# Kernel optimization log

Hardware: AMD Instinct MI355X
Metric: run time of the kernel (lower is better)

## Reference

```python
import jax, jax.numpy as jnp
import numpy as np

N_NODES = 100000
N_EDGES = 1200000
IN_DIM = 64
HID = 64
N_GRAPHS = 512
N_CLASSES = 1
LN_EPS = 1e-5
NORM_EPS = 1e-12


def _layer_norm(x, g, b):
    mu = x.mean(-1, keepdims=True)
    var = ((x - mu) ** 2).mean(-1, keepdims=True)
    return (x - mu) * jax.lax.rsqrt(var + LN_EPS) * g + b


def setup_inputs() -> dict:
    key = jax.random.key(0)
    ks = jax.random.split(key, 20)
    h = jax.random.normal(ks[0], (N_NODES, IN_DIM), jnp.float32)
    src = jax.random.randint(ks[1], (N_EDGES,), 0, N_NODES)
    dst = jax.random.randint(ks[2], (N_EDGES,), 0, N_NODES)
    graph_ids = jnp.sort(jax.random.randint(ks[3], (N_NODES,), 0, N_GRAPHS))
    s1 = 1.0 / np.sqrt(IN_DIM)
    s2 = 1.0 / np.sqrt(HID)
    s3 = 1.0 / np.sqrt(2 * HID)
    return {
        "h": h, "src": src, "dst": dst, "graph_ids": graph_ids,
        "W1": jax.random.normal(ks[4], (IN_DIM, HID), jnp.float32) * s1,
        "b1": jnp.zeros((HID,), jnp.float32),
        "W2": jax.random.normal(ks[5], (HID, HID), jnp.float32) * s2,
        "b2": jnp.zeros((HID,), jnp.float32),
        "g1": jnp.ones((HID,), jnp.float32), "be1": jnp.zeros((HID,), jnp.float32),
        "g2": jnp.ones((HID,), jnp.float32), "be2": jnp.zeros((HID,), jnp.float32),
        "g3": jnp.ones((HID,), jnp.float32), "be3": jnp.zeros((HID,), jnp.float32),
        "g4": jnp.ones((HID,), jnp.float32), "be4": jnp.zeros((HID,), jnp.float32),
        "Wc1": jax.random.normal(ks[6], (2 * HID, HID), jnp.float32) * s3,
        "bc1": jnp.zeros((HID,), jnp.float32),
        "Wc2": jax.random.normal(ks[7], (HID, HID), jnp.float32) * s2,
        "bc2": jnp.zeros((HID,), jnp.float32),
        "Wc3": jax.random.normal(ks[8], (HID, N_CLASSES), jnp.float32) * s2,
        "bc3": jnp.zeros((N_CLASSES,), jnp.float32),
    }


def reference(h, src, dst, graph_ids, W1, b1, W2, b2, g1, be1, g2, be2,
              g3, be3, g4, be4, Wc1, bc1, Wc2, bc2, Wc3, bc3):
    N = N_NODES
    ones_e = jnp.ones((src.shape[0],), jnp.float32)
    # DGL GraphConv norm='both': symmetric degree normalization (clamp 0 -> 1)
    deg_out = jnp.clip(jax.ops.segment_sum(ones_e, src, num_segments=N), 1.0)
    deg_in = jnp.clip(jax.ops.segment_sum(ones_e, dst, num_segments=N), 1.0)
    ns = (deg_out ** -0.5)[:, None]
    nd = (deg_in ** -0.5)[:, None]

    def conv(x, W, b):
        msg = (x * ns)[src]                                  # [E, d] gather
        agg = jax.ops.segment_sum(msg, dst, num_segments=N)  # [N, d] scatter-add
        return (agg * nd) @ W + b

    h1 = jax.nn.relu(_layer_norm(conv(h, W1, b1), g1, be1))
    h1 = jax.nn.relu(_layer_norm(conv(h1, W2, b2), g2, be2))

    # per-graph mean / max pooling (dgl.mean_nodes / dgl.max_nodes)
    ssum = jax.ops.segment_sum(h1, graph_ids, num_segments=N_GRAPHS)
    cnt = jnp.clip(jax.ops.segment_sum(jnp.ones((N,), jnp.float32), graph_ids,
                                       num_segments=N_GRAPHS), 1.0)
    hg = ssum / cnt[:, None]
    hg_max = jax.ops.segment_max(h1, graph_ids, num_segments=N_GRAPHS)

    def l2norm(x):  # F.normalize(p=2, dim=1)
        n = jnp.sqrt((x * x).sum(-1, keepdims=True))
        return x / jnp.maximum(n, NORM_EPS)

    hg = jnp.concatenate([l2norm(hg), l2norm(hg_max)], axis=1)  # [G, 2*HID]
    out = jax.nn.relu(_layer_norm(hg @ Wc1 + bc1, g3, be3))
    out = jax.nn.relu(_layer_norm(out @ Wc2 + bc2, g4, be4))
    return out @ Wc3 + bc3
```

## Files before the change

kernel.cpp:

```cpp
#include <hip/hip_runtime.h>
#include <math.h>

#define HID 64
#define LN_EPS 1e-5f
#define NORM_EPS 1e-12f
#define CHUNK 1024
#define CONV_BLOCKS 2048

typedef _Float16 half4v __attribute__((ext_vector_type(4)));

__device__ __forceinline__ float wave_sum64(float v) {
#pragma unroll
    for (int o = 32; o > 0; o >>= 1) v += __shfl_xor(v, o, 64);
    return v;
}

__device__ __forceinline__ int lower_bound_dev(const int* __restrict__ a, int n, int key) {
    int lo = 0, hi = n;
    while (lo < hi) {
        int mid = (lo + hi) >> 1;
        if (a[mid] < key) lo = mid + 1; else hi = mid;
    }
    return lo;
}

__global__ __launch_bounds__(256) void count_kernel(const int* __restrict__ src,
                                                    const int* __restrict__ dst,
                                                    int* __restrict__ cnt_out,
                                                    int* __restrict__ cnt_in,
                                                    int E) {
    int e0 = (blockIdx.x * 256 + threadIdx.x) * 4;
    if (e0 + 3 < E) {
        int4 s4 = *reinterpret_cast<const int4*>(src + e0);
        int4 d4 = *reinterpret_cast<const int4*>(dst + e0);
        atomicAdd(&cnt_out[s4.x], 1); atomicAdd(&cnt_out[s4.y], 1);
        atomicAdd(&cnt_out[s4.z], 1); atomicAdd(&cnt_out[s4.w], 1);
        atomicAdd(&cnt_in[d4.x], 1);  atomicAdd(&cnt_in[d4.y], 1);
        atomicAdd(&cnt_in[d4.z], 1);  atomicAdd(&cnt_in[d4.w], 1);
    } else {
        for (int e = e0; e < E; ++e) {
            atomicAdd(&cnt_out[src[e]], 1);
            atomicAdd(&cnt_in[dst[e]], 1);
        }
    }
}

__global__ __launch_bounds__(256) void scan1_kernel(const int* __restrict__ cnt_in,
                                                    const int* __restrict__ cnt_out,
                                                    float* __restrict__ ns,
                                                    float* __restrict__ nd,
                                                    int* __restrict__ cs,
                                                    int* __restrict__ partials,
                                                    int N) {
    __shared__ int wsum[4];
    int t = threadIdx.x;
    int lane = t & 63, wave = t >> 6;
    int base = blockIdx.x * CHUNK + t * 4;
    int v0 = (base + 0 < N) ? cnt_in[base + 0] : 0;
    int v1 = (base + 1 < N) ? cnt_in[base + 1] : 0;
    int v2 = (base + 2 < N) ? cnt_in[base + 2] : 0;
    int v3 = (base + 3 < N) ? cnt_in[base + 3] : 0;

    if (base + 3 < N) {
        int4 co = *reinterpret_cast<const int4*>(cnt_out + base);
        float4 nsv = make_float4(rsqrtf((float)max(co.x, 1)), rsqrtf((float)max(co.y, 1)),
                                 rsqrtf((float)max(co.z, 1)), rsqrtf((float)max(co.w, 1)));
        float4 ndv = make_float4(rsqrtf((float)max(v0, 1)), rsqrtf((float)max(v1, 1)),
                                 rsqrtf((float)max(v2, 1)), rsqrtf((float)max(v3, 1)));
        *reinterpret_cast<float4*>(ns + base) = nsv;
        *reinterpret_cast<float4*>(nd + base) = ndv;
    } else {
        for (int i = base; i < N; ++i) {
            ns[i] = rsqrtf((float)max(cnt_out[i], 1));
            nd[i] = rsqrtf((float)max(cnt_in[i], 1));
        }
    }

    int tsum = v0 + v1 + v2 + v3;
    int x = tsum;
#pragma unroll
    for (int off = 1; off < 64; off <<= 1) {
        int y = __shfl_up(x, off, 64);
        if (lane >= off) x += y;
    }
    if (lane == 63) wsum[wave] = x;
    __syncthreads();
    int waveoff = 0;
    for (int w = 0; w < wave; ++w) waveoff += wsum[w];
    int off0 = waveoff + x - tsum;
    if (base + 0 < N) cs[base + 0] = off0;
    if (base + 1 < N) cs[base + 1] = off0 + v0;
    if (base + 2 < N) cs[base + 2] = off0 + v0 + v1;
    if (base + 3 < N) cs[base + 3] = off0 + v0 + v1 + v2;
    if (t == 255) partials[blockIdx.x] = waveoff + x;
}

__global__ __launch_bounds__(256) void scan2_kernel(int* __restrict__ partials, int nch) {
    __shared__ int wsum[4];
    int t = threadIdx.x;
    int lane = t & 63, wave = t >> 6;
    int base = t * 4;
    int v0 = (base + 0 < nch) ? partials[base + 0] : 0;
    int v1 = (base + 1 < nch) ? partials[base + 1] : 0;
    int v2 = (base + 2 < nch) ? partials[base + 2] : 0;
    int v3 = (base + 3 < nch) ? partials[base + 3] : 0;
    int tsum = v0 + v1 + v2 + v3;
    int x = tsum;
#pragma unroll
    for (int off = 1; off < 64; off <<= 1) {
        int y = __shfl_up(x, off, 64);
        if (lane >= off) x += y;
    }
    if (lane == 63) wsum[wave] = x;
    __syncthreads();
    int waveoff = 0;
    for (int w = 0; w < wave; ++w) waveoff += wsum[w];
    int off0 = waveoff + x - tsum;
    if (base + 0 < nch) partials[base + 0] = off0;
    if (base + 1 < nch) partials[base + 1] = off0 + v0;
    if (base + 2 < nch) partials[base + 2] = off0 + v0 + v1;
    if (base + 3 < nch) partials[base + 3] = off0 + v0 + v1 + v2;
}

__global__ __launch_bounds__(256) void scan3_kernel(int* __restrict__ cs,
                                                    const int* __restrict__ partials,
                                                    int* __restrict__ cursor,
                                                    int N, int E) {
    int n = blockIdx.x * 256 + threadIdx.x;
    if (n < N) {
        int v = cs[n] + partials[n / CHUNK];
        cs[n] = v;
        cursor[n] = v;
    }
    if (n == 0) cs[N] = E;
}

__global__ __launch_bounds__(256) void prescale_kernel(const float* __restrict__ x,
                                                       const float* __restrict__ ns,
                                                       _Float16* __restrict__ xs,
                                                       int total) {
    int i = (blockIdx.x * 256 + threadIdx.x) * 4;
    if (i >= total) return;
    float w = ns[i >> 6];
    float4 v = *reinterpret_cast<const float4*>(x + i);
    half4v o;
    o.x = (_Float16)(v.x * w);
    o.y = (_Float16)(v.y * w);
    o.z = (_Float16)(v.z * w);
    o.w = (_Float16)(v.w * w);
    *reinterpret_cast<half4v*>(xs + i) = o;
}

__global__ __launch_bounds__(256) void fill_kernel(const int* __restrict__ src,
                                                   const int* __restrict__ dst,
                                                   int* __restrict__ cursor,
                                                   int* __restrict__ eidx,
                                                   int E) {
    int e0 = (blockIdx.x * 256 + threadIdx.x) * 4;
    if (e0 + 3 < E) {
        int4 s4 = *reinterpret_cast<const int4*>(src + e0);
        int4 d4 = *reinterpret_cast<const int4*>(dst + e0);
        int p0 = atomicAdd(&cursor[d4.x], 1);
        int p1 = atomicAdd(&cursor[d4.y], 1);
        int p2 = atomicAdd(&cursor[d4.z], 1);
        int p3 = atomicAdd(&cursor[d4.w], 1);
        eidx[p0] = s4.x;
        eidx[p1] = s4.y;
        eidx[p2] = s4.z;
        eidx[p3] = s4.w;
    } else {
        for (int e = e0; e < E; ++e) {
            int p = atomicAdd(&cursor[dst[e]], 1);
            eidx[p] = src[e];
        }
    }
}

template <int MODE>
__global__ __launch_bounds__(256, 8) void conv_kernel(const _Float16* __restrict__ xs,
                                                      const int* __restrict__ eidx,
                                                      const int* __restrict__ cs,
                                                      const float* __restrict__ nd,
                                                      const float* __restrict__ ns,
                                                      const float* __restrict__ W,
                                                      const float* __restrict__ b,
                                                      const float* __restrict__ gam,
                                                      const float* __restrict__ bet,
                                                      void* __restrict__ outp,
                                                      int N) {
    __shared__ float Ws[HID * HID];
    int tid = threadIdx.x;
#pragma unroll
    for (int i = tid; i < HID * HID / 4; i += 256) {
        reinterpret_cast<float4*>(Ws)[i] = reinterpret_cast<const float4*>(W)[i];
    }
    __syncthreads();
    int wave = tid >> 6;
    int lane = tid & 63;
    float bl = b[lane], gl = gam[lane], bel = bet[lane];

    for (int n = blockIdx.x * 4 + wave; n < N; n += CONV_BLOCKS * 4) {
        int beg = cs[n], end = cs[n + 1];
        float acc = 0.0f;
        int e = beg;
        for (; e + 4 <= end; e += 4) {
            int s0 = eidx[e + 0];
            int s1 = eidx[e + 1];
            int s2 = eidx[e + 2];
            int s3 = eidx[e + 3];
            float v0 = (float)xs[(size_t)s0 * HID + lane];
            float v1 = (float)xs[(size_t)s1 * HID + lane];
            float v2 = (float)xs[(size_t)s2 * HID + lane];
            float v3 = (float)xs[(size_t)s3 * HID + lane];
            acc += (v0 + v1) + (v2 + v3);
        }
        for (; e < end; ++e) {
            acc += (float)xs[(size_t)eidx[e] * HID + lane];
        }
        float t = acc * nd[n];

        float y = bl;
#pragma unroll 8
        for (int k = 0; k < HID; ++k) {
            y = fmaf(__shfl(t, k, 64), Ws[k * HID + lane], y);
        }
        float mu = wave_sum64(y) * (1.0f / HID);
        float d = y - mu;
        float var = wave_sum64(d * d) * (1.0f / HID);
        float o = d * rsqrtf(var + LN_EPS) * gl + bel;
        o = fmaxf(o, 0.0f);
        if (MODE == 1) {
            ((_Float16*)outp)[(size_t)n * HID + lane] = (_Float16)(o * ns[n]);
        } else {
            ((float*)outp)[(size_t)n * HID + lane] = o;
        }
    }
}

__global__ __launch_bounds__(256) void pool_kernel(const float* __restrict__ h1,
                                                   const int* __restrict__ gid,
                                                   float* __restrict__ gsum,
                                                   float* __restrict__ gmaxf,
                                                   float* __restrict__ gcnt,
                                                   int N) {
    __shared__ float psum[4][HID];
    __shared__ float pmax[4][HID];
    __shared__ int se[2];
    int g = blockIdx.x;
    int tid = threadIdx.x;
    if (tid == 0) se[0] = lower_bound_dev(gid, N, g);
    if (tid == 64) se[1] = lower_bound_dev(gid, N, g + 1);
    __syncthreads();
    int s = se[0], e = se[1];
    int wave = tid >> 6, lane = tid & 63;
    float sum = 0.0f, mx = 0.0f;
    for (int r = s + wave; r < e; r += 4) {
        float v = h1[(size_t)r * HID + lane];
        sum += v;
        mx = fmaxf(mx, v);
    }
    psum[wave][lane] = sum;
    pmax[wave][lane] = mx;
    __syncthreads();
    if (tid < HID) {
        float ts = psum[0][tid] + psum[1][tid] + psum[2][tid] + psum[3][tid];
        float tm = fmaxf(fmaxf(pmax[0][tid], pmax[1][tid]), fmaxf(pmax[2][tid], pmax[3][tid]));
        gsum[(size_t)g * HID + tid] = ts;
        gmaxf[(size_t)g * HID + tid] = tm;
        if (tid == 0) gcnt[g] = (float)(e - s);
    }
}

__global__ __launch_bounds__(64) void head_kernel(const float* __restrict__ gsum,
                                                  const float* __restrict__ gmaxf,
                                                  const float* __restrict__ gcnt,
                                                  const float* __restrict__ Wc1,
                                                  const float* __restrict__ bc1,
                                                  const float* __restrict__ g3,
                                                  const float* __restrict__ be3,
                                                  const float* __restrict__ Wc2,
                                                  const float* __restrict__ bc2,
                                                  const float* __restrict__ g4,
                                                  const float* __restrict__ be4,
                                                  const float* __restrict__ Wc3,
                                                  const float* __restrict__ bc3,
                                                  float* __restrict__ out) {
    __shared__ float hg[2 * HID];
    __shared__ float t1[HID];
    int g = blockIdx.x;
    int lane = threadIdx.x;

    float cnt = fmaxf(gcnt[g], 1.0f);
    float mean = gsum[(size_t)g * HID + lane] / cnt;
    float mx = gmaxf[(size_t)g * HID + lane];

    float s1 = sqrtf(wave_sum64(mean * mean));
    float a = mean / fmaxf(s1, NORM_EPS);
    float s2 = sqrtf(wave_sum64(mx * mx));
    float bmx = mx / fmaxf(s2, NORM_EPS);

    hg[lane] = a;
    hg[HID + lane] = bmx;
    __syncthreads();

    float y = bc1[lane];
#pragma unroll 8
    for (int k = 0; k < 2 * HID; ++k) {
        y = fmaf(hg[k], Wc1[k * HID + lane], y);
    }
    float mu = wave_sum64(y) * (1.0f / HID);
    float d = y - mu;
    float var = wave_sum64(d * d) * (1.0f / HID);
    float o = d * rsqrtf(var + LN_EPS) * g3[lane] + be3[lane];
    o = fmaxf(o, 0.0f);
    t1[lane] = o;
    __syncthreads();

    float y2 = bc2[lane];
#pragma unroll 8
    for (int k = 0; k < HID; ++k) {
        y2 = fmaf(t1[k], Wc2[k * HID + lane], y2);
    }
    mu = wave_sum64(y2) * (1.0f / HID);
    d = y2 - mu;
    var = wave_sum64(d * d) * (1.0f / HID);
    o = d * rsqrtf(var + LN_EPS) * g4[lane] + be4[lane];
    o = fmaxf(o, 0.0f);

    float v = o * Wc3[lane];
    v = wave_sum64(v);
    if (lane == 0) out[g] = v + bc3[0];
}

extern "C" void kernel_launch(void* const* d_in, const int* in_sizes, int n_in,
                              void* d_out, int out_size, void* d_ws, size_t ws_size,
                              hipStream_t stream) {
    const float* h   = (const float*)d_in[0];
    const int*   src = (const int*)d_in[1];
    const int*   dst = (const int*)d_in[2];
    const int*   gid = (const int*)d_in[3];
    const float* W1  = (const float*)d_in[4];
    const float* b1  = (const float*)d_in[5];
    const float* W2  = (const float*)d_in[6];
    const float* b2  = (const float*)d_in[7];
    const float* g1  = (const float*)d_in[8];
    const float* be1 = (const float*)d_in[9];
    const float* g2  = (const float*)d_in[10];
    const float* be2 = (const float*)d_in[11];
    const float* g3  = (const float*)d_in[12];
    const float* be3 = (const float*)d_in[13];
    const float* g4  = (const float*)d_in[14];
    const float* be4 = (const float*)d_in[15];
    const float* Wc1 = (const float*)d_in[16];
    const float* bc1 = (const float*)d_in[17];
    const float* Wc2 = (const float*)d_in[18];
    const float* bc2 = (const float*)d_in[19];
    const float* Wc3 = (const float*)d_in[20];
    const float* bc3 = (const float*)d_in[21];
    float* out = (float*)d_out;

    const int N = in_sizes[0] / HID;
    const int E = in_sizes[1];
    const int G = out_size;

    char* ws = (char*)d_ws;
    _Float16* xs1 = (_Float16*)ws;
    _Float16* xs2 = xs1 + (size_t)N * HID;
    float* h2     = (float*)(xs2 + (size_t)N * HID);
    int*   eidx   = (int*)(h2 + (size_t)N * HID);
    float* ns     = (float*)(eidx + E);
    float* nd     = ns + N;
    int*   cnt_out= (int*)(nd + N);
    int*   cnt_in = cnt_out + N;
    int*   cs     = cnt_in + N;
    int*   partials = cs + N + 4;
    float* gsum   = (float*)(partials + 1024);
    float* gmaxf  = gsum + (size_t)G * HID;
    float* gcnt   = gmaxf + (size_t)G * HID;

    const int nch = (N + CHUNK - 1) / CHUNK;
    const int E4 = (E + 3) / 4;
    const int total = N * HID;

    hipMemsetAsync(cnt_out, 0, sizeof(int) * (size_t)2 * N, stream);

    count_kernel<<<(E4 + 255) / 256, 256, 0, stream>>>(src, dst, cnt_out, cnt_in, E);
    scan1_kernel<<<nch, 256, 0, stream>>>(cnt_in, cnt_out, ns, nd, cs, partials, N);
    scan2_kernel<<<1, 256, 0, stream>>>(partials, nch);
    scan3_kernel<<<(N + 255) / 256, 256, 0, stream>>>(cs, partials, cnt_out, N, E);
    prescale_kernel<<<(total / 4 + 255) / 256, 256, 0, stream>>>(h, ns, xs1, total);
    fill_kernel<<<(E4 + 255) / 256, 256, 0, stream>>>(src, dst, cnt_out, eidx, E);

    conv_kernel<1><<<CONV_BLOCKS, 256, 0, stream>>>(xs1, eidx, cs, nd, ns, W1, b1, g1, be1, xs2, N);
    conv_kernel<0><<<CONV_BLOCKS, 256, 0, stream>>>(xs2, eidx, cs, nd, ns, W2, b2, g2, be2, h2, N);

    pool_kernel<<<G, 256, 0, stream>>>(h2, gid, gsum, gmaxf, gcnt, N);

    head_kernel<<<G, 64, 0, stream>>>(gsum, gmaxf, gcnt, Wc1, bc1, g3, be3,
                                      Wc2, bc2, g4, be4, Wc3, bc3, out);
}
```

Baseline: 577.2 us.

## Store final conv output in fp16, add nontemporal hints, simplify edge kernels

The second conv layer now writes its output as fp16 with nontemporal stores, and the pooling kernel reads that fp16 buffer, halving the bytes written and read for h2. Edge-index loads in the conv gather use nontemporal loads. The count and fill kernels drop the 4-edges-per-thread int4 vectorisation in favour of one edge per thread. Storing h2 in fp16 reduces the precision of pooled features, and the scalar edge kernels issue more, narrower loads.

```diff
diff --git a/kernel.cpp b/kernel.cpp
--- a/kernel.cpp
+++ b/kernel.cpp
@@ -29,20 +29,10 @@
                                                     int* __restrict__ cnt_out,
                                                     int* __restrict__ cnt_in,
                                                     int E) {
-    int e0 = (blockIdx.x * 256 + threadIdx.x) * 4;
-    if (e0 + 3 < E) {
-        int4 s4 = *reinterpret_cast<const int4*>(src + e0);
-        int4 d4 = *reinterpret_cast<const int4*>(dst + e0);
-        atomicAdd(&cnt_out[s4.x], 1); atomicAdd(&cnt_out[s4.y], 1);
-        atomicAdd(&cnt_out[s4.z], 1); atomicAdd(&cnt_out[s4.w], 1);
-        atomicAdd(&cnt_in[d4.x], 1);  atomicAdd(&cnt_in[d4.y], 1);
-        atomicAdd(&cnt_in[d4.z], 1);  atomicAdd(&cnt_in[d4.w], 1);
-    } else {
-        for (int e = e0; e < E; ++e) {
-            atomicAdd(&cnt_out[src[e]], 1);
-            atomicAdd(&cnt_in[dst[e]], 1);
-        }
-    }
+    int e = blockIdx.x * 256 + threadIdx.x;
+    if (e >= E) return;
+    atomicAdd(&cnt_out[src[e]], 1);
+    atomicAdd(&cnt_in[dst[e]], 1);
 }
 
 __global__ __launch_bounds__(256) void scan1_kernel(const int* __restrict__ cnt_in,
@@ -156,24 +146,10 @@
                                                    int* __restrict__ cursor,
                                                    int* __restrict__ eidx,
                                                    int E) {
-    int e0 = (blockIdx.x * 256 + threadIdx.x) * 4;
-    if (e0 + 3 < E) {
-        int4 s4 = *reinterpret_cast<const int4*>(src + e0);
-        int4 d4 = *reinterpret_cast<const int4*>(dst + e0);
-        int p0 = atomicAdd(&cursor[d4.x], 1);
-        int p1 = atomicAdd(&cursor[d4.y], 1);
-        int p2 = atomicAdd(&cursor[d4.z], 1);
-        int p3 = atomicAdd(&cursor[d4.w], 1);
-        eidx[p0] = s4.x;
-        eidx[p1] = s4.y;
-        eidx[p2] = s4.z;
-        eidx[p3] = s4.w;
-    } else {
-        for (int e = e0; e < E; ++e) {
-            int p = atomicAdd(&cursor[dst[e]], 1);
-            eidx[p] = src[e];
-        }
-    }
+    int e = blockIdx.x * 256 + threadIdx.x;
+    if (e >= E) return;
+    int p = atomicAdd(&cursor[dst[e]], 1);
+    eidx[p] = src[e];
 }
 
 template <int MODE>
@@ -186,7 +162,7 @@
                                                       const float* __restrict__ b,
                                                       const float* __restrict__ gam,
                                                       const float* __restrict__ bet,
-                                                      void* __restrict__ outp,
+                                                      _Float16* __restrict__ outp,
                                                       int N) {
     __shared__ float Ws[HID * HID];
     int tid = threadIdx.x;
@@ -204,10 +180,10 @@
         float acc = 0.0f;
         int e = beg;
         for (; e + 4 <= end; e += 4) {
-            int s0 = eidx[e + 0];
-            int s1 = eidx[e + 1];
-            int s2 = eidx[e + 2];
-            int s3 = eidx[e + 3];
+            int s0 = __builtin_nontemporal_load(eidx + e + 0);
+            int s1 = __builtin_nontemporal_load(eidx + e + 1);
+            int s2 = __builtin_nontemporal_load(eidx + e + 2);
+            int s3 = __builtin_nontemporal_load(eidx + e + 3);
             float v0 = (float)xs[(size_t)s0 * HID + lane];
             float v1 = (float)xs[(size_t)s1 * HID + lane];
             float v2 = (float)xs[(size_t)s2 * HID + lane];
@@ -215,7 +191,8 @@
             acc += (v0 + v1) + (v2 + v3);
         }
         for (; e < end; ++e) {
-            acc += (float)xs[(size_t)eidx[e] * HID + lane];
+            int s = __builtin_nontemporal_load(eidx + e);
+            acc += (float)xs[(size_t)s * HID + lane];
         }
         float t = acc * nd[n];
 
@@ -230,14 +207,14 @@
         float o = d * rsqrtf(var + LN_EPS) * gl + bel;
         o = fmaxf(o, 0.0f);
         if (MODE == 1) {
-            ((_Float16*)outp)[(size_t)n * HID + lane] = (_Float16)(o * ns[n]);
+            outp[(size_t)n * HID + lane] = (_Float16)(o * ns[n]);
         } else {
-            ((float*)outp)[(size_t)n * HID + lane] = o;
-        }
-    }
-}
-
-__global__ __launch_bounds__(256) void pool_kernel(const float* __restrict__ h1,
+            __builtin_nontemporal_store((_Float16)o, &outp[(size_t)n * HID + lane]);
+        }
+    }
+}
+
+__global__ __launch_bounds__(256) void pool_kernel(const _Float16* __restrict__ h1,
                                                    const int* __restrict__ gid,
                                                    float* __restrict__ gsum,
                                                    float* __restrict__ gmaxf,
@@ -255,7 +232,7 @@
     int wave = tid >> 6, lane = tid & 63;
     float sum = 0.0f, mx = 0.0f;
     for (int r = s + wave; r < e; r += 4) {
-        float v = h1[(size_t)r * HID + lane];
+        float v = (float)h1[(size_t)r * HID + lane];
         sum += v;
         mx = fmaxf(mx, v);
     }
@@ -366,7 +343,7 @@
     char* ws = (char*)d_ws;
     _Float16* xs1 = (_Float16*)ws;
     _Float16* xs2 = xs1 + (size_t)N * HID;
-    float* h2     = (float*)(xs2 + (size_t)N * HID);
+    _Float16* h2  = xs2 + (size_t)N * HID;
     int*   eidx   = (int*)(h2 + (size_t)N * HID);
     float* ns     = (float*)(eidx + E);
     float* nd     = ns + N;
@@ -379,20 +356,19 @@
     float* gcnt   = gmaxf + (size_t)G * HID;
 
     const int nch = (N + CHUNK - 1) / CHUNK;
-    const int E4 = (E + 3) / 4;
     const int total = N * HID;
 
     hipMemsetAsync(cnt_out, 0, sizeof(int) * (size_t)2 * N, stream);
 
-    count_kernel<<<(E4 + 255) / 256, 256, 0, stream>>>(src, dst, cnt_out, cnt_in, E);
+    count_kernel<<<(E + 255) / 256, 256, 0, stream>>>(src, dst, cnt_out, cnt_in, E);
     scan1_kernel<<<nch, 256, 0, stream>>>(cnt_in, cnt_out, ns, nd, cs, partials, N);
     scan2_kernel<<<1, 256, 0, stream>>>(partials, nch);
     scan3_kernel<<<(N + 255) / 256, 256, 0, stream>>>(cs, partials, cnt_out, N, E);
     prescale_kernel<<<(total / 4 + 255) / 256, 256, 0, stream>>>(h, ns, xs1, total);
-    fill_kernel<<<(E4 + 255) / 256, 256, 0, stream>>>(src, dst, cnt_out, eidx, E);
+    fill_kernel<<<(E + 255) / 256, 256, 0, stream>>>(src, dst, cnt_out, eidx, E);
 
     conv_kernel<1><<<CONV_BLOCKS, 256, 0, stream>>>(xs1, eidx, cs, nd, ns, W1, b1, g1, be1, xs2, N);
-    conv_kernel<0><<<CONV_BLOCKS, 256, 0, stream>>>(xs2, eidx, cs, nd, ns, W2, b2, g2, be2, h2, N);
+    conv_kernel<2><<<CONV_BLOCKS, 256, 0, stream>>>(xs2, eidx, cs, nd, ns, W2, b2, g2, be2, h2, N);
 
     pool_kernel<<<G, 256, 0, stream>>>(h2, gid, gsum, gmaxf, gcnt, N);
 
```

New measurement: 591.8 us. 1.03x slower.
